# Performance work log

Hardware: AMD Instinct MI355X
Metric: run time of the kernel (lower is better)

## Reference

```python
import jax, jax.numpy as jnp
import numpy as np
from jax import lax

B, N, D = 2, 4096, 4
CHUNK = 256
GLOBAL_COUPLING = 1.0
STEP_SIZE = 1.0
GAMMA_STRENGTH = 1.0
EPS = 1e-6


def setup_inputs() -> dict:
    key = jax.random.key(0)
    k1, k2, k3, k4 = jax.random.split(key, 4)
    return {
        "theta_prev": jax.random.normal(k1, (B, N, D), dtype=jnp.float32),
        "gamma_prev": jax.random.normal(k2, (B, N, D), dtype=jnp.float32),
        "theta_connectivity_weight": jax.random.uniform(k3, (B, N, N), dtype=jnp.float32),
        "alpha_t": jax.random.normal(k4, (B, N, N), dtype=jnp.float32),
    }


def _coupling(theta_prev, W, alpha):
    # Chunked all-pairs Kuramoto coupling, faithful to the torch chunk loop
    # (eval mode: alpha_t used as given).
    b, n, d = theta_prev.shape
    nc = n // CHUNK
    # chunk-major stacking of the i axis: [nc, B, CHUNK, ...]
    ti = theta_prev.reshape(b, nc, CHUNK, d).transpose(1, 0, 2, 3)
    Wc = W.reshape(b, nc, CHUNK, n).transpose(1, 0, 2, 3)
    ac = alpha.reshape(b, nc, CHUNK, n).transpose(1, 0, 2, 3)

    def body(carry, x):
        ti_c, W_c, a_c = x  # [B,CHUNK,D], [B,CHUNK,N], [B,CHUNK,N]
        # phase[b,i,j,d] = sin(theta_j - theta_i - alpha_ij)
        phase = jnp.sin(theta_prev[:, None, :, :] - ti_c[:, :, None, :] - a_c[..., None])
        out = jnp.einsum('bin,bind->bid', W_c, phase)  # sum over j
        return carry, out

    _, chunks = lax.scan(body, None, (ti, Wc, ac))  # [nc, B, CHUNK, D]
    coupling = chunks.transpose(1, 0, 2, 3).reshape(b, n, d)
    return (GLOBAL_COUPLING / float(n)) * coupling


def reference(theta_prev, gamma_prev, theta_connectivity_weight, alpha_t):
    coupling = _coupling(theta_prev, theta_connectivity_weight, alpha_t)
    drive = GAMMA_STRENGTH * (gamma_prev - theta_prev)
    theta_next = theta_prev + STEP_SIZE * (drive + coupling)
    # F.normalize(dim=-1, eps=1e-6): x / max(||x||_2, eps)
    norm = jnp.sqrt(jnp.sum(theta_next * theta_next, axis=-1, keepdims=True))
    return theta_next / jnp.maximum(norm, EPS)
```

## Files before the change

kernel.cpp:

```cpp
#include <hip/hip_runtime.h>
#include <math.h>

constexpr int kN = 4096;
constexpr int kD = 4;
constexpr int kB = 2;
constexpr int kBlock = 256;
constexpr int kRowsPerWave = 4;
constexpr int kWaves = kBlock / 64;
constexpr int kRowsPerBlock = kRowsPerWave * kWaves;
constexpr int kIters = kN / (64 * 4);

__global__ __launch_bounds__(256)
void table_kernel(const float* __restrict__ theta,
                  float4* __restrict__ sinT, float4* __restrict__ cosT)
{
    const int idx = blockIdx.x * blockDim.x + threadIdx.x;
    const float4 t4 = *reinterpret_cast<const float4*>(&theta[(size_t)idx * kD]);
    float4 s4, c4;
    __sincosf(t4.x, &s4.x, &c4.x);
    __sincosf(t4.y, &s4.y, &c4.y);
    __sincosf(t4.z, &s4.z, &c4.z);
    __sincosf(t4.w, &s4.w, &c4.w);
    sinT[idx] = s4;
    cosT[idx] = c4;
}

template <bool USE_TABLE>
__global__ __launch_bounds__(kBlock)
void kuramoto_kernel(const float* __restrict__ theta,
                     const float* __restrict__ gam,
                     const float* __restrict__ W,
                     const float* __restrict__ alpha,
                     const float4* __restrict__ sinT,
                     const float4* __restrict__ cosT,
                     float* __restrict__ out)
{
    const int tid  = threadIdx.x;
    const int wave = tid >> 6;
    const int lane = tid & 63;

    const int row0 = blockIdx.x * kRowsPerBlock + wave * kRowsPerWave;
    const int b    = row0 >> 12;

    const float* Wr[kRowsPerWave];
    const float* Ar[kRowsPerWave];
    #pragma unroll
    for (int r = 0; r < kRowsPerWave; ++r) {
        Wr[r] = W     + (size_t)(row0 + r) * kN;
        Ar[r] = alpha + (size_t)(row0 + r) * kN;
    }
    const float4* __restrict__ sB = sinT + (size_t)b * kN;
    const float4* __restrict__ cB = cosT + (size_t)b * kN;
    const float* thetaB = theta + (size_t)b * kN * kD;

    float U[kRowsPerWave][kD];
    float V[kRowsPerWave][kD];
    #pragma unroll
    for (int r = 0; r < kRowsPerWave; ++r)
        #pragma unroll
        for (int d = 0; d < kD; ++d) { U[r][d] = 0.f; V[r][d] = 0.f; }

    auto load_stage = [&](int k, float4 (&s)[4], float4 (&c)[4],
                          float4 (&w)[4], float4 (&a)[4]) {
        const int jb = k * 256 + lane * 4;
        #pragma unroll
        for (int u = 0; u < 4; ++u) {
            if constexpr (USE_TABLE) {
                s[u] = sB[jb + u];
                c[u] = cB[jb + u];
            } else {
                s[u] = *reinterpret_cast<const float4*>(&thetaB[(size_t)(jb + u) * kD]);
            }
        }
        #pragma unroll
        for (int r = 0; r < kRowsPerWave; ++r) {
            w[r] = *reinterpret_cast<const float4*>(&Wr[r][jb]);
            a[r] = *reinterpret_cast<const float4*>(&Ar[r][jb]);
        }
    };

    auto compute_stage = [&](const float4 (&s)[4], const float4 (&c)[4],
                             const float4 (&w)[4], const float4 (&a)[4]) {
        float sv[4][kD], cv[4][kD];
        #pragma unroll
        for (int u = 0; u < 4; ++u) {
            if constexpr (USE_TABLE) {
                sv[u][0] = s[u].x; sv[u][1] = s[u].y; sv[u][2] = s[u].z; sv[u][3] = s[u].w;
                cv[u][0] = c[u].x; cv[u][1] = c[u].y; cv[u][2] = c[u].z; cv[u][3] = c[u].w;
            } else {
                __sincosf(s[u].x, &sv[u][0], &cv[u][0]);
                __sincosf(s[u].y, &sv[u][1], &cv[u][1]);
                __sincosf(s[u].z, &sv[u][2], &cv[u][2]);
                __sincosf(s[u].w, &sv[u][3], &cv[u][3]);
            }
        }
        #pragma unroll
        for (int r = 0; r < kRowsPerWave; ++r) {
            const float wv[4] = {w[r].x, w[r].y, w[r].z, w[r].w};
            const float av[4] = {a[r].x, a[r].y, a[r].z, a[r].w};
            #pragma unroll
            for (int u = 0; u < 4; ++u) {
                float sa, ca;
                __sincosf(av[u], &sa, &ca);
                const float P = wv[u] * ca;
                const float Q = wv[u] * sa;
                U[r][0] = fmaf(P, sv[u][0], fmaf(-Q, cv[u][0], U[r][0]));
                V[r][0] = fmaf(P, cv[u][0], fmaf( Q, sv[u][0], V[r][0]));
                U[r][1] = fmaf(P, sv[u][1], fmaf(-Q, cv[u][1], U[r][1]));
                V[r][1] = fmaf(P, cv[u][1], fmaf( Q, sv[u][1], V[r][1]));
                U[r][2] = fmaf(P, sv[u][2], fmaf(-Q, cv[u][2], U[r][2]));
                V[r][2] = fmaf(P, cv[u][2], fmaf( Q, sv[u][2], V[r][2]));
                U[r][3] = fmaf(P, sv[u][3], fmaf(-Q, cv[u][3], U[r][3]));
                V[r][3] = fmaf(P, cv[u][3], fmaf( Q, sv[u][3], V[r][3]));
            }
        }
    };

    float4 sA[4], cA[4], wA[4], aA[4];
    float4 sX[4], cX[4], wX[4], aX[4];

    load_stage(0, sA, cA, wA, aA);
    for (int k = 0; k < kIters - 2; k += 2) {
        load_stage(k + 1, sX, cX, wX, aX);
        __builtin_amdgcn_sched_barrier(0);
        compute_stage(sA, cA, wA, aA);
        load_stage(k + 2, sA, cA, wA, aA);
        __builtin_amdgcn_sched_barrier(0);
        compute_stage(sX, cX, wX, aX);
    }
    load_stage(kIters - 1, sX, cX, wX, aX);
    __builtin_amdgcn_sched_barrier(0);
    compute_stage(sA, cA, wA, aA);
    compute_stage(sX, cX, wX, aX);

    #pragma unroll
    for (int m = 1; m < 64; m <<= 1) {
        #pragma unroll
        for (int r = 0; r < kRowsPerWave; ++r)
            #pragma unroll
            for (int d = 0; d < kD; ++d) {
                U[r][d] += __shfl_xor(U[r][d], m, 64);
                V[r][d] += __shfl_xor(V[r][d], m, 64);
            }
    }

    #pragma unroll
    for (int r = 0; r < kRowsPerWave; ++r) {
        if (lane == r) {
            const int row = row0 + r;
            const float4 t4 = *reinterpret_cast<const float4*>(&theta[(size_t)row * kD]);
            const float4 g4 = *reinterpret_cast<const float4*>(&gam[(size_t)row * kD]);
            const float tv[4] = {t4.x, t4.y, t4.z, t4.w};
            const float gv[4] = {g4.x, g4.y, g4.z, g4.w};
            constexpr float scale = 1.0f / (float)kN;
            float x[4];
            float nsq = 0.f;
            #pragma unroll
            for (int d = 0; d < kD; ++d) {
                float si, ci;
                __sincosf(tv[d], &si, &ci);
                const float coup = scale * (ci * U[r][d] - si * V[r][d]);
                x[d] = gv[d] + coup;
                nsq += x[d] * x[d];
            }
            const float inv = 1.0f / fmaxf(sqrtf(nsq), 1e-6f);
            float4 o;
            o.x = x[0] * inv; o.y = x[1] * inv; o.z = x[2] * inv; o.w = x[3] * inv;
            *reinterpret_cast<float4*>(&out[(size_t)row * kD]) = o;
        }
    }
}

extern "C" void kernel_launch(void* const* d_in, const int* in_sizes, int n_in,
                              void* d_out, int out_size, void* d_ws, size_t ws_size,
                              hipStream_t stream) {
    const float* theta = (const float*)d_in[0];
    const float* gam   = (const float*)d_in[1];
    const float* W     = (const float*)d_in[2];
    const float* alpha = (const float*)d_in[3];
    float* out = (float*)d_out;

    const int totalRows = in_sizes[0] / kD;
    const int nblocks = totalRows / kRowsPerBlock;
    const size_t tabEntries = (size_t)kB * kN;
    const size_t needWs = 2 * tabEntries * sizeof(float4);

    if (ws_size >= needWs) {
        float4* sinT = (float4*)d_ws;
        float4* cosT = sinT + tabEntries;
        table_kernel<<<(int)(tabEntries / 256), 256, 0, stream>>>(theta, sinT, cosT);
        kuramoto_kernel<true><<<nblocks, kBlock, 0, stream>>>(
            theta, gam, W, alpha, sinT, cosT, out);
    } else {
        kuramoto_kernel<false><<<nblocks, kBlock, 0, stream>>>(
            theta, gam, W, alpha, nullptr, nullptr, out);
    }
}
```

Baseline: 51.50 us.

## Split the j reduction across two waves per row group and combine via shared memory

Each block now covers 8 rows instead of 16. Within a block, pairs of waves split the j dimension in half, and the partial U/V sums are combined through shared memory after a block barrier. This doubles the grid size and halves the serial loop length per wave, to raise occupancy and memory-level parallelism on this bandwidth-heavy kernel. The cost is an extra __syncthreads, a small shared-memory reduction, and half the waves sitting idle during the epilogue.

After: 67.33 us. 1.31x slower.

```diff
diff --git a/kernel.cpp b/kernel.cpp
--- a/kernel.cpp
+++ b/kernel.cpp
@@ -6,9 +6,11 @@
 constexpr int kB = 2;
 constexpr int kBlock = 256;
 constexpr int kRowsPerWave = 4;
-constexpr int kWaves = kBlock / 64;
-constexpr int kRowsPerBlock = kRowsPerWave * kWaves;
-constexpr int kIters = kN / (64 * 4);
+constexpr int kJSplit = 2;
+constexpr int kRowGroups = 2;
+constexpr int kRowsPerBlock = kRowsPerWave * kRowGroups;
+constexpr int kJPerWave = kN / kJSplit;
+constexpr int kIters = kJPerWave / 256;
 
 __global__ __launch_bounds__(256)
 void table_kernel(const float* __restrict__ theta,
@@ -35,23 +37,28 @@
                      const float4* __restrict__ cosT,
                      float* __restrict__ out)
 {
+    __shared__ float sRed[kRowGroups][kJSplit][kRowsPerWave][kD][2];
+
     const int tid  = threadIdx.x;
     const int wave = tid >> 6;
     const int lane = tid & 63;
-
-    const int row0 = blockIdx.x * kRowsPerBlock + wave * kRowsPerWave;
-    const int b    = row0 >> 12;
+    const int rg   = wave >> 1;
+    const int jh   = wave & 1;
+
+    const int row0  = blockIdx.x * kRowsPerBlock + rg * kRowsPerWave;
+    const int b     = row0 >> 12;
+    const int jbase = jh * kJPerWave;
 
     const float* Wr[kRowsPerWave];
     const float* Ar[kRowsPerWave];
     #pragma unroll
     for (int r = 0; r < kRowsPerWave; ++r) {
-        Wr[r] = W     + (size_t)(row0 + r) * kN;
-        Ar[r] = alpha + (size_t)(row0 + r) * kN;
-    }
-    const float4* __restrict__ sB = sinT + (size_t)b * kN;
-    const float4* __restrict__ cB = cosT + (size_t)b * kN;
-    const float* thetaB = theta + (size_t)b * kN * kD;
+        Wr[r] = W     + (size_t)(row0 + r) * kN + jbase;
+        Ar[r] = alpha + (size_t)(row0 + r) * kN + jbase;
+    }
+    const float4* __restrict__ sB = sinT + (size_t)b * kN + jbase;
+    const float4* __restrict__ cB = cosT + (size_t)b * kN + jbase;
+    const float* thetaB = theta + ((size_t)b * kN + jbase) * kD;
 
     float U[kRowsPerWave][kD];
     float V[kRowsPerWave][kD];
@@ -144,29 +151,44 @@
             }
     }
 
-    #pragma unroll
-    for (int r = 0; r < kRowsPerWave; ++r) {
-        if (lane == r) {
-            const int row = row0 + r;
-            const float4 t4 = *reinterpret_cast<const float4*>(&theta[(size_t)row * kD]);
-            const float4 g4 = *reinterpret_cast<const float4*>(&gam[(size_t)row * kD]);
-            const float tv[4] = {t4.x, t4.y, t4.z, t4.w};
-            const float gv[4] = {g4.x, g4.y, g4.z, g4.w};
-            constexpr float scale = 1.0f / (float)kN;
-            float x[4];
-            float nsq = 0.f;
+    if (lane == 0) {
+        #pragma unroll
+        for (int r = 0; r < kRowsPerWave; ++r)
             #pragma unroll
             for (int d = 0; d < kD; ++d) {
-                float si, ci;
-                __sincosf(tv[d], &si, &ci);
-                const float coup = scale * (ci * U[r][d] - si * V[r][d]);
-                x[d] = gv[d] + coup;
-                nsq += x[d] * x[d];
-            }
-            const float inv = 1.0f / fmaxf(sqrtf(nsq), 1e-6f);
-            float4 o;
-            o.x = x[0] * inv; o.y = x[1] * inv; o.z = x[2] * inv; o.w = x[3] * inv;
-            *reinterpret_cast<float4*>(&out[(size_t)row * kD]) = o;
+                sRed[rg][jh][r][d][0] = U[r][d];
+                sRed[rg][jh][r][d][1] = V[r][d];
+            }
+    }
+    __syncthreads();
+
+    if (jh == 0) {
+        #pragma unroll
+        for (int r = 0; r < kRowsPerWave; ++r) {
+            if (lane == r) {
+                const int row = row0 + r;
+                const float4 t4 = *reinterpret_cast<const float4*>(&theta[(size_t)row * kD]);
+                const float4 g4 = *reinterpret_cast<const float4*>(&gam[(size_t)row * kD]);
+                const float tv[4] = {t4.x, t4.y, t4.z, t4.w};
+                const float gv[4] = {g4.x, g4.y, g4.z, g4.w};
+                constexpr float scale = 1.0f / (float)kN;
+                float x[4];
+                float nsq = 0.f;
+                #pragma unroll
+                for (int d = 0; d < kD; ++d) {
+                    const float Uf = U[r][d] + sRed[rg][1][r][d][0];
+                    const float Vf = V[r][d] + sRed[rg][1][r][d][1];
+                    float si, ci;
+                    __sincosf(tv[d], &si, &ci);
+                    const float coup = scale * (ci * Uf - si * Vf);
+                    x[d] = gv[d] + coup;
+                    nsq += x[d] * x[d];
+                }
+                const float inv = 1.0f / fmaxf(sqrtf(nsq), 1e-6f);
+                float4 o;
+                o.x = x[0] * inv; o.y = x[1] * inv; o.z = x[2] * inv; o.w = x[3] * inv;
+                *reinterpret_cast<float4*>(&out[(size_t)row * kD]) = o;
+            }
         }
     }
 }
```
